# Optimization experiments

Hardware: AMD Instinct MI355X
Metric: run time of the kernel (lower is better)

The kernel has to match this reference:

```python
import jax, jax.numpy as jnp
import numpy as np
import math

B, N, E, F_IN, H = 16, 2048, 32768, 32, 128
RATIO = 0.8
K1 = math.ceil(RATIO * N)      # 1639
K2 = math.ceil(RATIO * K1)     # 1312
K3 = math.ceil(RATIO * K2)     # 1050


def setup_inputs() -> dict:
    key = jax.random.key(0)
    ks = jax.random.split(key, 20)

    def lin(k, out_d, in_d):
        s = 1.0 / np.sqrt(in_d)
        return jax.random.uniform(k, (out_d, in_d), minval=-s, maxval=s, dtype=jnp.float32)

    return {
        "x": jax.random.normal(ks[0], (B, N, F_IN), dtype=jnp.float32),
        "edge_index": jax.random.randint(ks[1], (B, 2, E), 0, N, dtype=jnp.int32),
        "W_root1": lin(ks[2], H, F_IN), "W_rel1": lin(ks[3], H, F_IN), "b1": jnp.zeros((H,), jnp.float32),
        "p1": jax.random.normal(ks[4], (H,), dtype=jnp.float32) * 0.1,
        "W_root2": lin(ks[5], H, H), "W_rel2": lin(ks[6], H, H), "b2": jnp.zeros((H,), jnp.float32),
        "p2": jax.random.normal(ks[7], (H,), dtype=jnp.float32) * 0.1,
        "W_root3": lin(ks[8], H, H), "W_rel3": lin(ks[9], H, H), "b3": jnp.zeros((H,), jnp.float32),
        "p3": jax.random.normal(ks[10], (H,), dtype=jnp.float32) * 0.1,
        "lin1_W": lin(ks[11], 128, 256), "lin1_b": jnp.zeros((128,), jnp.float32),
        "lin2_W": lin(ks[12], 64, 128), "lin2_b": jnp.zeros((64,), jnp.float32),
        "lin3_W": lin(ks[13], 1, 64), "lin3_b": jnp.zeros((1,), jnp.float32),
    }


def _graph_conv(x, src, dst, ev, W_rel, b, W_root):
    # GraphConv: out_i = W_root x_i + W_rel * sum_{j->i} x_j + b
    n = x.shape[0]
    msg = x[src] * ev[:, None].astype(x.dtype)            # [E, F] gather
    agg = jnp.zeros((n, x.shape[1]), x.dtype).at[dst].add(msg)  # scatter-add
    return agg @ W_rel.T + b + x @ W_root.T


def _topk_pool(x, src, dst, ev, p, k):
    # TopKPooling: score = tanh(x.p/||p||); keep top-k nodes; x' = x[perm]*score[perm]
    score = jnp.tanh((x @ p) / jnp.linalg.norm(p))        # [n]
    vals, perm = jax.lax.top_k(score, k)
    x_new = x[perm] * vals[:, None]
    inv = jnp.full((x.shape[0],), -1, jnp.int32).at[perm].set(jnp.arange(k, dtype=jnp.int32))
    ns, nd = inv[src], inv[dst]
    valid = ev & (ns >= 0) & (nd >= 0)
    return x_new, jnp.where(valid, ns, 0), jnp.where(valid, nd, 0), valid


def _readout(x):
    # cat([global_max_pool, global_mean_pool])
    return jnp.concatenate([x.max(axis=0), x.mean(axis=0)])


def reference(x, edge_index,
              W_root1, W_rel1, b1, p1,
              W_root2, W_rel2, b2, p2,
              W_root3, W_rel3, b3, p3,
              lin1_W, lin1_b, lin2_W, lin2_b, lin3_W, lin3_b):
    def per_graph(xg, eg):
        src, dst = eg[0], eg[1]
        ev = jnp.ones((E,), bool)
        h = jax.nn.relu(_graph_conv(xg, src, dst, ev, W_rel1, b1, W_root1))
        h, src, dst, ev = _topk_pool(h, src, dst, ev, p1, K1)
        r1 = _readout(h)
        h = jax.nn.relu(_graph_conv(h, src, dst, ev, W_rel2, b2, W_root2))
        h, src, dst, ev = _topk_pool(h, src, dst, ev, p2, K2)
        r2 = _readout(h)
        h = jax.nn.relu(_graph_conv(h, src, dst, ev, W_rel3, b3, W_root3))
        h, src, dst, ev = _topk_pool(h, src, dst, ev, p3, K3)
        r3 = _readout(h)
        return r1 + r2 + r3                                # [256]

    g = jax.vmap(per_graph)(x, edge_index)                 # [B, 256]
    h = jax.nn.relu(g @ lin1_W.T + lin1_b)
    h = jax.nn.relu(h @ lin2_W.T + lin2_b)
    out = jax.nn.sigmoid(h @ lin3_W.T + lin3_b)            # [B, 1]
    return out[:, 0]
```

## Files before the change

### kernel.cpp

```cpp
#include <hip/hip_runtime.h>
#include <cstdint>
#include <math.h>

#define BB 16
#define NN 2048
#define EE 32768
#define FIN 32
#define HH 128
#define KK1 1639
#define KK2 1312
#define KK3 1050
#define PARTS 128
#define PGRP 8
#define JPG (PARTS / PGRP)
#define DEGC 64

using f16x8 = __attribute__((ext_vector_type(8))) _Float16;
using f16x2 = __attribute__((ext_vector_type(2))) _Float16;
using f32x4 = __attribute__((ext_vector_type(4))) float;

__global__ void wcvt_kernel(const float* __restrict__ Wr1, const float* __restrict__ Wl1,
                            const float* __restrict__ Wr2, const float* __restrict__ Wl2,
                            const float* __restrict__ Wr3, const float* __restrict__ Wl3,
                            _Float16* __restrict__ wcat1, _Float16* __restrict__ wcat2,
                            _Float16* __restrict__ wcat3) {
    int idx = blockIdx.x * 256 + threadIdx.x;
    if (idx < 128 * 64) {
        int col = idx >> 6, k = idx & 63;
        float v = (k < FIN) ? Wr1[col * FIN + k] : Wl1[col * FIN + (k - FIN)];
        wcat1[idx] = (_Float16)v;
    } else if (idx < 128 * 64 + 128 * 256) {
        int i2 = idx - 128 * 64;
        int col = i2 >> 8, k = i2 & 255;
        float v = (k < HH) ? Wr2[col * HH + k] : Wl2[col * HH + (k - HH)];
        wcat2[i2] = (_Float16)v;
    } else {
        int i3 = idx - 128 * 64 - 128 * 256;
        if (i3 < 128 * 256) {
            int col = i3 >> 8, k = i3 & 255;
            float v = (k < HH) ? Wr3[col * HH + k] : Wl3[col * HH + (k - HH)];
            wcat3[i3] = (_Float16)v;
        }
    }
}

__global__ void build1_kernel(const int* __restrict__ ei,
                              int* __restrict__ deg, int* __restrict__ csr) {
    int t = blockIdx.x * blockDim.x + threadIdx.x;
    int e = t & (EE - 1);
    int b = t >> 15;
    if (b >= BB) return;
    int s = ei[(size_t)b * 2 * EE + e];
    int d = ei[(size_t)b * 2 * EE + EE + e];
    int pos = atomicAdd(&deg[b * NN + d], 1);
    if (pos < DEGC) csr[((size_t)b * NN + d) * DEGC + pos] = s;
}

__global__ __launch_bounds__(256) void agg1_csr_kernel(
    const float* __restrict__ x, const int* __restrict__ deg,
    const int* __restrict__ csr, _Float16* __restrict__ agg) {
    int b = blockIdx.x;
    int g = threadIdx.x >> 5, lane = threadIdx.x & 31;
    int node = blockIdx.y * 8 + g;
    int dg = deg[b * NN + node]; if (dg > DEGC) dg = DEGC;
    const int* bucket = csr + ((size_t)b * NN + node) * DEGC;
    float acc = 0.f;
    for (int base = 0; base < dg; base += 16) {
        int m = dg - base; if (m > 16) m = 16;
        int myidx = (lane < m) ? bucket[base + lane] : 0;
        float v[16];
        int idx[16];
#pragma unroll
        for (int u = 0; u < 16; u++) idx[u] = __shfl(myidx, u, 32);
#pragma unroll
        for (int u = 0; u < 16; u++)
            v[u] = x[((size_t)b * NN + idx[u]) * FIN + lane];
#pragma unroll
        for (int u = 0; u < 16; u++)
            acc += (u < m) ? v[u] : 0.f;
    }
    agg[((size_t)b * NN + node) * FIN + lane] = (_Float16)acc;
}

__global__ __launch_bounds__(256) void agg23_csr_kernel(
    const _Float16* __restrict__ x, const int* __restrict__ deg,
    const int* __restrict__ csr, _Float16* __restrict__ agg, int n) {
    int b = blockIdx.x;
    int wv = threadIdx.x >> 6, lane = threadIdx.x & 63;
    int node = blockIdx.y * 4 + wv;
    if (node >= n) return;
    int dg = deg[b * NN + node]; if (dg > DEGC) dg = DEGC;
    const int* bucket = csr + ((size_t)b * NN + node) * DEGC;
    const f16x2* xf2 = reinterpret_cast<const f16x2*>(x);
    float ax = 0.f, ay = 0.f;
    for (int base = 0; base < dg; base += 16) {
        int m = dg - base; if (m > 16) m = 16;
        int myidx = (lane < m) ? bucket[base + lane] : 0;
        int idx[16];
#pragma unroll
        for (int u = 0; u < 16; u++) idx[u] = __shfl(myidx, u);
        f16x2 v[16];
#pragma unroll
        for (int u = 0; u < 16; u++)
            v[u] = xf2[((size_t)b * NN + idx[u]) * 64 + lane];
#pragma unroll
        for (int u = 0; u < 16; u++) {
            ax += (u < m) ? (float)v[u][0] : 0.f;
            ay += (u < m) ? (float)v[u][1] : 0.f;
        }
    }
    f16x2 o; o[0] = (_Float16)ax; o[1] = (_Float16)ay;
    reinterpret_cast<f16x2*>(agg)[((size_t)b * NN + node) * 64 + lane] = o;
}

__device__ __forceinline__ f16x8 load_cvt16(const float* src) {
    float4 lo = *reinterpret_cast<const float4*>(src);
    float4 hi = *reinterpret_cast<const float4*>(src + 4);
    f16x8 r;
    r[0] = (_Float16)lo.x; r[1] = (_Float16)lo.y;
    r[2] = (_Float16)lo.z; r[3] = (_Float16)lo.w;
    r[4] = (_Float16)hi.x; r[5] = (_Float16)hi.y;
    r[6] = (_Float16)hi.z; r[7] = (_Float16)hi.w;
    return r;
}

template<int FI, bool XF32>
__global__ __launch_bounds__(256) void conv_mfma_kernel(
    const void* __restrict__ xv, const _Float16* __restrict__ ah,
    const _Float16* __restrict__ wcat,
    const float* __restrict__ bias, const float* __restrict__ p,
    _Float16* __restrict__ h, unsigned long long* __restrict__ keys,
    float* __restrict__ ssc, int n) {
    __shared__ float spart[4][32];
    __shared__ float snorm_s;
    const float* xf = (const float*)xv;
    const _Float16* xh = (const _Float16*)xv;
    int b = blockIdx.x;
    int r0 = blockIdx.y * 32;
    int t = threadIdx.x;
    int wv = t >> 6, lane = t & 63;
    int m16 = lane & 15, q = lane >> 4;

    if (t < 64) {
        float v = p[t] * p[t] + p[t + 64] * p[t + 64];
#pragma unroll
        for (int off = 32; off; off >>= 1) v += __shfl_xor(v, off);
        if (t == 0) snorm_s = sqrtf(v);
    }

    f32x4 acc[2][2];
#pragma unroll
    for (int rt = 0; rt < 2; rt++)
#pragma unroll
        for (int ct = 0; ct < 2; ct++) {
            acc[rt][ct][0] = 0.f; acc[rt][ct][1] = 0.f;
            acc[rt][ct][2] = 0.f; acc[rt][ct][3] = 0.f;
        }

    int rowA[2] = { r0 + m16, r0 + 16 + m16 };
    int colB[2] = { wv * 32 + m16, wv * 32 + 16 + m16 };

#pragma unroll
    for (int step = 0; step < (2 * FI) / 32; step++) {
        int k0 = step * 32 + q * 8;
        f16x8 afr[2], bfr[2];
#pragma unroll
        for (int rt = 0; rt < 2; rt++) {
            if (k0 < FI) {
                if constexpr (XF32)
                    afr[rt] = load_cvt16(xf + ((size_t)b * NN + rowA[rt]) * FI + k0);
                else
                    afr[rt] = *reinterpret_cast<const f16x8*>(
                        xh + ((size_t)b * NN + rowA[rt]) * FI + k0);
            } else {
                afr[rt] = *reinterpret_cast<const f16x8*>(
                    ah + ((size_t)b * NN + rowA[rt]) * FI + (k0 - FI));
            }
        }
#pragma unroll
        for (int ct = 0; ct < 2; ct++)
            bfr[ct] = *reinterpret_cast<const f16x8*>(
                wcat + (size_t)colB[ct] * (2 * FI) + k0);
#pragma unroll
        for (int rt = 0; rt < 2; rt++)
#pragma unroll
            for (int ct = 0; ct < 2; ct++)
                acc[rt][ct] = __builtin_amdgcn_mfma_f32_16x16x32_f16(
                    afr[rt], bfr[ct], acc[rt][ct], 0, 0, 0);
    }

    float prt[2][4];
#pragma unroll
    for (int rt = 0; rt < 2; rt++)
#pragma unroll
        for (int reg = 0; reg < 4; reg++) prt[rt][reg] = 0.f;

#pragma unroll
    for (int ct = 0; ct < 2; ct++) {
        int col = wv * 32 + ct * 16 + m16;
        float pc = p[col];
        float bv = bias[col];
#pragma unroll
        for (int rt = 0; rt < 2; rt++)
#pragma unroll
            for (int reg = 0; reg < 4; reg++) {
                int row = r0 + rt * 16 + q * 4 + reg;
                float hv = fmaxf(acc[rt][ct][reg] + bv, 0.f);
                if (row < n)
                    h[((size_t)b * NN + row) * HH + col] = (_Float16)hv;
                prt[rt][reg] += hv * pc;
            }
    }
#pragma unroll
    for (int rt = 0; rt < 2; rt++)
#pragma unroll
        for (int reg = 0; reg < 4; reg++) {
            float v = prt[rt][reg];
            v += __shfl_xor(v, 1); v += __shfl_xor(v, 2);
            v += __shfl_xor(v, 4); v += __shfl_xor(v, 8);
            prt[rt][reg] = v;
        }
    if (m16 == 0) {
#pragma unroll
        for (int rt = 0; rt < 2; rt++)
#pragma unroll
            for (int reg = 0; reg < 4; reg++)
                spart[wv][rt * 16 + q * 4 + reg] = prt[rt][reg];
    }
    __syncthreads();
    if (t < 32) {
        int row = r0 + t;
        if (row < n) {
            float s = spart[0][t] + spart[1][t] + spart[2][t] + spart[3][t];
            float sc = tanhf(s / snorm_s);
            unsigned u = __float_as_uint(sc);
            u = (u & 0x80000000u) ? ~u : (u ^ 0x80000000u);
            u = ~u;
            keys[(size_t)b * NN + row] = ((unsigned long long)u << 32) | (unsigned)row;
            ssc[(size_t)b * NN + row] = sc;
        }
    }
}

__global__ __launch_bounds__(256) void rank_kernel(
    const unsigned long long* __restrict__ keys, const float* __restrict__ ssc,
    int n, int k, int* __restrict__ perm, float* __restrict__ vals,
    int* __restrict__ inv) {
    __shared__ unsigned long long sk[NN];
    __shared__ int pr2[256];
    int b = blockIdx.x;
    for (int i = threadIdx.x; i < NN; i += 256)
        sk[i] = (i < n) ? keys[(size_t)b * NN + i] : ~0ULL;
    __syncthreads();
    int il = threadIdx.x & 63;
    int jg = threadIdx.x >> 6;
    int i = blockIdx.y * 64 + il;
    unsigned long long my = sk[i];
    int rank = 0;
#pragma unroll 8
    for (int j = jg * 512; j < jg * 512 + 512; j++)
        rank += (sk[j] < my) ? 1 : 0;
    pr2[threadIdx.x] = rank;
    __syncthreads();
    if (jg == 0 && i < n) {
        rank = pr2[il] + pr2[64 + il] + pr2[128 + il] + pr2[192 + il];
        if (rank < k) {
            perm[b * NN + rank] = i;
            vals[b * NN + rank] = ssc[(size_t)b * NN + i];
            inv[b * NN + i] = rank;
        } else {
            inv[b * NN + i] = -1;
        }
    }
}

__global__ __launch_bounds__(256) void fat_gather_build_kernel(
    int nbuild,
    const int* __restrict__ inv,
    const int* __restrict__ sin_, const int* __restrict__ din_, int in_stride,
    int* __restrict__ sout, int* __restrict__ dout, int write_next,
    int* __restrict__ deg, int* __restrict__ csr,
    const _Float16* __restrict__ hin, _Float16* __restrict__ xout,
    const int* __restrict__ perm, const float* __restrict__ vals, int k,
    float* __restrict__ part) {
    if ((int)blockIdx.x < nbuild) {
        int t = blockIdx.x * 256 + threadIdx.x;
        int e = t & (EE - 1);
        int b = t >> 15;
        if (b >= BB) return;
        int s = sin_[(size_t)b * in_stride + e];
        int d = din_[(size_t)b * in_stride + e];
        int ns = -1, nd = -1;
        if (s >= 0 && d >= 0) {
            ns = inv[b * NN + s];
            nd = inv[b * NN + d];
        }
        if (ns < 0 || nd < 0) { ns = -1; nd = -1; }
        if (write_next) {
            sout[(size_t)b * EE + e] = ns;
            dout[(size_t)b * EE + e] = nd;
        }
        if (nd >= 0) {
            int pos = atomicAdd(&deg[b * NN + nd], 1);
            if (pos < DEGC) csr[((size_t)b * NN + nd) * DEGC + pos] = ns;
        }
    } else {
        int gblk = blockIdx.x - nbuild;
        int pair = gblk * 2 + (threadIdx.x >> 7);
        int b = pair & 15;
        int j = pair >> 4;
        int f = threadIdx.x & 127;
        float mx = -INFINITY, sm = 0.f;
        int i = j;
        int pi = (i < k) ? perm[b * NN + i] : 0;
        float v = (i < k) ? vals[b * NN + i] : 0.f;
        while (i < k) {
            int inext = i + PARTS;
            int pin = 0; float vn = 0.f;
            if (inext < k) { pin = perm[b * NN + inext]; vn = vals[b * NN + inext]; }
            float hv = (float)hin[((size_t)b * NN + pi) * HH + f] * v;
            xout[((size_t)b * NN + i) * HH + f] = (_Float16)hv;
            mx = fmaxf(mx, hv);
            sm += hv;
            i = inext; pi = pin; v = vn;
        }
        part[((size_t)b * PARTS + j) * 256 + f] = mx;
        part[((size_t)b * PARTS + j) * 256 + 128 + f] = sm;
    }
}

__global__ __launch_bounds__(256) void combine_kernel(
    const float* __restrict__ partAll, float* __restrict__ partG) {
    int blk = blockIdx.x;
    int g = blk % PGRP;
    int rem = blk / PGRP;
    int b = rem & 15;
    int l = rem >> 4;
    int f = threadIdx.x;
    const float* src = partAll + ((((size_t)l * BB + b) * PARTS) + (size_t)g * JPG) * 256;
    float r;
    if (f < 128) {
        r = -INFINITY;
#pragma unroll
        for (int j = 0; j < JPG; j++) r = fmaxf(r, src[j * 256 + f]);
    } else {
        r = 0.f;
#pragma unroll
        for (int j = 0; j < JPG; j++) r += src[j * 256 + f];
    }
    partG[(((size_t)l * BB + b) * PGRP + g) * 256 + f] = r;
}

__global__ __launch_bounds__(256) void mlp_kernel(
    const float* __restrict__ partG,
    const float* __restrict__ W1, const float* __restrict__ b1,
    const float* __restrict__ W2, const float* __restrict__ b2,
    const float* __restrict__ W3, const float* __restrict__ b3,
    float* __restrict__ out) {
    __shared__ float sg[256];
    __shared__ float s1[128];
    __shared__ float s2[64];
    int b = blockIdx.x, tid = threadIdx.x;
    const float kk[3] = {(float)KK1, (float)KK2, (float)KK3};
    float acc = 0.f;
    if (tid < 128) {
#pragma unroll
        for (int l = 0; l < 3; l++) {
            float mx = -INFINITY;
#pragma unroll
            for (int j = 0; j < PGRP; j++)
                mx = fmaxf(mx, partG[(((size_t)l * BB + b) * PGRP + j) * 256 + tid]);
            acc += mx;
        }
    } else {
#pragma unroll
        for (int l = 0; l < 3; l++) {
            float sm = 0.f;
#pragma unroll
            for (int j = 0; j < PGRP; j++)
                sm += partG[(((size_t)l * BB + b) * PGRP + j) * 256 + tid];
            acc += sm / kk[l];
        }
    }
    sg[tid] = acc;
    __syncthreads();
    if (tid < 128) {
        float a = b1[tid];
        for (int j = 0; j < 256; j++) a += sg[j] * W1[tid * 256 + j];
        s1[tid] = fmaxf(a, 0.f);
    }
    __syncthreads();
    if (tid < 64) {
        float a = b2[tid];
        for (int j = 0; j < 128; j++) a += s1[j] * W2[tid * 128 + j];
        s2[tid] = fmaxf(a, 0.f);
    }
    __syncthreads();
    if (tid == 0) {
        float a = b3[0];
        for (int j = 0; j < 64; j++) a += s2[j] * W3[j];
        out[b] = 1.f / (1.f + expf(-a));
    }
}

extern "C" void kernel_launch(void* const* d_in, const int* in_sizes, int n_in,
                              void* d_out, int out_size, void* d_ws, size_t ws_size,
                              hipStream_t stream) {
    const float* x   = (const float*)d_in[0];
    const int*   ei  = (const int*)d_in[1];
    const float* Wr1 = (const float*)d_in[2];
    const float* Wl1 = (const float*)d_in[3];
    const float* b1  = (const float*)d_in[4];
    const float* p1  = (const float*)d_in[5];
    const float* Wr2 = (const float*)d_in[6];
    const float* Wl2 = (const float*)d_in[7];
    const float* b2  = (const float*)d_in[8];
    const float* p2  = (const float*)d_in[9];
    const float* Wr3 = (const float*)d_in[10];
    const float* Wl3 = (const float*)d_in[11];
    const float* b3  = (const float*)d_in[12];
    const float* p3  = (const float*)d_in[13];
    const float* l1W = (const float*)d_in[14];
    const float* l1b = (const float*)d_in[15];
    const float* l2W = (const float*)d_in[16];
    const float* l2b = (const float*)d_in[17];
    const float* l3W = (const float*)d_in[18];
    const float* l3b = (const float*)d_in[19];
    float* out = (float*)d_out;

    char* ws = (char*)d_ws;
    _Float16* bufA = (_Float16*)ws; ws += (size_t)BB * NN * HH * 2;
    _Float16* bufB = (_Float16*)ws; ws += (size_t)BB * NN * HH * 2;
    _Float16* agg  = (_Float16*)ws; ws += (size_t)BB * NN * HH * 2;
    int*   perm = (int*)ws;   ws += (size_t)BB * NN * 4;
    float* vals = (float*)ws; ws += (size_t)BB * NN * 4;
    int*   inv  = (int*)ws;   ws += (size_t)BB * NN * 4;
    int*   curS = (int*)ws;   ws += (size_t)BB * EE * 4;
    int*   curD = (int*)ws;   ws += (size_t)BB * EE * 4;
    float* partAll = (float*)ws; ws += (size_t)3 * BB * PARTS * 256 * 4;
    float* partG   = (float*)ws; ws += (size_t)3 * BB * PGRP * 256 * 4;
    int*   deg1 = (int*)ws;   ws += (size_t)BB * NN * 4;
    int*   deg2 = (int*)ws;   ws += (size_t)BB * NN * 4;
    int*   deg3 = (int*)ws;   ws += (size_t)BB * NN * 4;
    int*   csr  = (int*)ws;   ws += (size_t)BB * NN * DEGC * 4;
    unsigned long long* keys = (unsigned long long*)ws; ws += (size_t)BB * NN * 8;
    float* ssc  = (float*)ws; ws += (size_t)BB * NN * 4;
    _Float16* wcat1 = (_Float16*)ws; ws += (size_t)128 * 64 * 2;
    _Float16* wcat2 = (_Float16*)ws; ws += (size_t)128 * 256 * 2;
    _Float16* wcat3 = (_Float16*)ws; ws += (size_t)128 * 256 * 2;
    float* part1 = partAll;
    float* part2 = partAll + (size_t)BB * PARTS * 256;
    float* part3 = partAll + (size_t)2 * BB * PARTS * 256;

    hipMemsetAsync(deg1, 0, (size_t)3 * BB * NN * 4, stream);
    hipLaunchKernelGGL(wcvt_kernel, dim3((128 * 64 + 2 * 128 * 256 + 255) / 256), dim3(256), 0, stream,
                       Wr1, Wl1, Wr2, Wl2, Wr3, Wl3, wcat1, wcat2, wcat3);

    hipLaunchKernelGGL(build1_kernel, dim3(BB * EE / 256), dim3(256), 0, stream, ei, deg1, csr);
    hipLaunchKernelGGL(agg1_csr_kernel, dim3(BB, NN / 8), dim3(256), 0, stream, x, deg1, csr, agg);
    hipLaunchKernelGGL((conv_mfma_kernel<FIN, true>), dim3(BB, NN / 32), dim3(256), 0, stream,
                       (const void*)x, agg, wcat1, b1, p1, bufA, keys, ssc, NN);
    hipLaunchKernelGGL(rank_kernel, dim3(BB, NN / 64), dim3(256), 0, stream, keys, ssc, NN, KK1, perm, vals, inv);
    hipLaunchKernelGGL(fat_gather_build_kernel, dim3(2048 + BB * PARTS / 2), dim3(256), 0, stream,
                       2048, inv, ei, ei + EE, 2 * EE, curS, curD, 1, deg2, csr,
                       bufA, bufB, perm, vals, KK1, part1);

    hipLaunchKernelGGL(agg23_csr_kernel, dim3(BB, (KK1 + 3) / 4), dim3(256), 0, stream, bufB, deg2, csr, agg, KK1);
    hipLaunchKernelGGL((conv_mfma_kernel<HH, false>), dim3(BB, (KK1 + 31) / 32), dim3(256), 0, stream,
                       (const void*)bufB, agg, wcat2, b2, p2, bufA, keys, ssc, KK1);
    hipLaunchKernelGGL(rank_kernel, dim3(BB, NN / 64), dim3(256), 0, stream, keys, ssc, KK1, KK2, perm, vals, inv);
    hipLaunchKernelGGL(fat_gather_build_kernel, dim3(2048 + BB * PARTS / 2), dim3(256), 0, stream,
                       2048, inv, curS, curD, EE, curS, curD, 0, deg3, csr,
                       bufA, bufB, perm, vals, KK2, part2);

    hipLaunchKernelGGL(agg23_csr_kernel, dim3(BB, (KK2 + 3) / 4), dim3(256), 0, stream, bufB, deg3, csr, agg, KK2);
    hipLaunchKernelGGL((conv_mfma_kernel<HH, false>), dim3(BB, (KK2 + 31) / 32), dim3(256), 0, stream,
                       (const void*)bufB, agg, wcat3, b3, p3, bufA, keys, ssc, KK2);
    hipLaunchKernelGGL(rank_kernel, dim3(BB, NN / 64), dim3(256), 0, stream, keys, ssc, KK2, KK3, perm, vals, inv);
    hipLaunchKernelGGL(fat_gather_build_kernel, dim3(BB * PARTS / 2), dim3(256), 0, stream,
                       0, inv, curS, curD, EE, curS, curD, 0, deg3, csr,
                       bufA, bufB, perm, vals, KK3, part3);

    hipLaunchKernelGGL(combine_kernel, dim3(3 * BB * PGRP), dim3(256), 0, stream, partAll, partG);
    hipLaunchKernelGGL(mlp_kernel, dim3(BB), dim3(256), 0, stream,
                       partG, l1W, l1b, l2W, l2b, l3W, l3b, out);
}
```

Measured before the change: 217.5 us.

## Fuse CSR aggregation into MFMA conv kernels and merge prep launches

Neighbour aggregation now runs inside the conv kernels and writes into shared memory instead of a global agg buffer, so the separate agg kernels and their global round trip go away. The weight conversion and CSR build are merged into one prep kernel, and the combine kernel is dropped, so the MLP kernel reduces all 128 partials directly. This cuts launch count and global traffic. In exchange, the conv blocks become serial gather-then-MFMA with fewer blocks doing the gather work, and the MLP kernel now runs a longer serial reduction with only 16 blocks.

```diff
diff --git a/kernel.cpp b/kernel.cpp
--- a/kernel.cpp
+++ b/kernel.cpp
@@ -11,106 +11,48 @@
 #define KK2 1312
 #define KK3 1050
 #define PARTS 128
-#define PGRP 8
-#define JPG (PARTS / PGRP)
 #define DEGC 64
 
 using f16x8 = __attribute__((ext_vector_type(8))) _Float16;
 using f16x2 = __attribute__((ext_vector_type(2))) _Float16;
 using f32x4 = __attribute__((ext_vector_type(4))) float;
 
-__global__ void wcvt_kernel(const float* __restrict__ Wr1, const float* __restrict__ Wl1,
+__global__ void prep_kernel(const int* __restrict__ ei,
+                            int* __restrict__ deg, int* __restrict__ csr,
+                            const float* __restrict__ Wr1, const float* __restrict__ Wl1,
                             const float* __restrict__ Wr2, const float* __restrict__ Wl2,
                             const float* __restrict__ Wr3, const float* __restrict__ Wl3,
                             _Float16* __restrict__ wcat1, _Float16* __restrict__ wcat2,
                             _Float16* __restrict__ wcat3) {
-    int idx = blockIdx.x * 256 + threadIdx.x;
-    if (idx < 128 * 64) {
-        int col = idx >> 6, k = idx & 63;
-        float v = (k < FIN) ? Wr1[col * FIN + k] : Wl1[col * FIN + (k - FIN)];
-        wcat1[idx] = (_Float16)v;
-    } else if (idx < 128 * 64 + 128 * 256) {
-        int i2 = idx - 128 * 64;
-        int col = i2 >> 8, k = i2 & 255;
-        float v = (k < HH) ? Wr2[col * HH + k] : Wl2[col * HH + (k - HH)];
-        wcat2[i2] = (_Float16)v;
+    if (blockIdx.x < 2048) {
+        int t = blockIdx.x * 256 + threadIdx.x;
+        int e = t & (EE - 1);
+        int b = t >> 15;
+        if (b >= BB) return;
+        int s = ei[(size_t)b * 2 * EE + e];
+        int d = ei[(size_t)b * 2 * EE + EE + e];
+        int pos = atomicAdd(&deg[b * NN + d], 1);
+        if (pos < DEGC) csr[((size_t)b * NN + d) * DEGC + pos] = s;
     } else {
-        int i3 = idx - 128 * 64 - 128 * 256;
-        if (i3 < 128 * 256) {
-            int col = i3 >> 8, k = i3 & 255;
-            float v = (k < HH) ? Wr3[col * HH + k] : Wl3[col * HH + (k - HH)];
-            wcat3[i3] = (_Float16)v;
-        }
-    }
-}
-
-__global__ void build1_kernel(const int* __restrict__ ei,
-                              int* __restrict__ deg, int* __restrict__ csr) {
-    int t = blockIdx.x * blockDim.x + threadIdx.x;
-    int e = t & (EE - 1);
-    int b = t >> 15;
-    if (b >= BB) return;
-    int s = ei[(size_t)b * 2 * EE + e];
-    int d = ei[(size_t)b * 2 * EE + EE + e];
-    int pos = atomicAdd(&deg[b * NN + d], 1);
-    if (pos < DEGC) csr[((size_t)b * NN + d) * DEGC + pos] = s;
-}
-
-__global__ __launch_bounds__(256) void agg1_csr_kernel(
-    const float* __restrict__ x, const int* __restrict__ deg,
-    const int* __restrict__ csr, _Float16* __restrict__ agg) {
-    int b = blockIdx.x;
-    int g = threadIdx.x >> 5, lane = threadIdx.x & 31;
-    int node = blockIdx.y * 8 + g;
-    int dg = deg[b * NN + node]; if (dg > DEGC) dg = DEGC;
-    const int* bucket = csr + ((size_t)b * NN + node) * DEGC;
-    float acc = 0.f;
-    for (int base = 0; base < dg; base += 16) {
-        int m = dg - base; if (m > 16) m = 16;
-        int myidx = (lane < m) ? bucket[base + lane] : 0;
-        float v[16];
-        int idx[16];
-#pragma unroll
-        for (int u = 0; u < 16; u++) idx[u] = __shfl(myidx, u, 32);
-#pragma unroll
-        for (int u = 0; u < 16; u++)
-            v[u] = x[((size_t)b * NN + idx[u]) * FIN + lane];
-#pragma unroll
-        for (int u = 0; u < 16; u++)
-            acc += (u < m) ? v[u] : 0.f;
-    }
-    agg[((size_t)b * NN + node) * FIN + lane] = (_Float16)acc;
-}
-
-__global__ __launch_bounds__(256) void agg23_csr_kernel(
-    const _Float16* __restrict__ x, const int* __restrict__ deg,
-    const int* __restrict__ csr, _Float16* __restrict__ agg, int n) {
-    int b = blockIdx.x;
-    int wv = threadIdx.x >> 6, lane = threadIdx.x & 63;
-    int node = blockIdx.y * 4 + wv;
-    if (node >= n) return;
-    int dg = deg[b * NN + node]; if (dg > DEGC) dg = DEGC;
-    const int* bucket = csr + ((size_t)b * NN + node) * DEGC;
-    const f16x2* xf2 = reinterpret_cast<const f16x2*>(x);
-    float ax = 0.f, ay = 0.f;
-    for (int base = 0; base < dg; base += 16) {
-        int m = dg - base; if (m > 16) m = 16;
-        int myidx = (lane < m) ? bucket[base + lane] : 0;
-        int idx[16];
-#pragma unroll
-        for (int u = 0; u < 16; u++) idx[u] = __shfl(myidx, u);
-        f16x2 v[16];
-#pragma unroll
-        for (int u = 0; u < 16; u++)
-            v[u] = xf2[((size_t)b * NN + idx[u]) * 64 + lane];
-#pragma unroll
-        for (int u = 0; u < 16; u++) {
-            ax += (u < m) ? (float)v[u][0] : 0.f;
-            ay += (u < m) ? (float)v[u][1] : 0.f;
-        }
-    }
-    f16x2 o; o[0] = (_Float16)ax; o[1] = (_Float16)ay;
-    reinterpret_cast<f16x2*>(agg)[((size_t)b * NN + node) * 64 + lane] = o;
+        int idx = (blockIdx.x - 2048) * 256 + threadIdx.x;
+        if (idx < 128 * 64) {
+            int col = idx >> 6, k = idx & 63;
+            float v = (k < FIN) ? Wr1[col * FIN + k] : Wl1[col * FIN + (k - FIN)];
+            wcat1[idx] = (_Float16)v;
+        } else if (idx < 128 * 64 + 128 * 256) {
+            int i2 = idx - 128 * 64;
+            int col = i2 >> 8, k = i2 & 255;
+            float v = (k < HH) ? Wr2[col * HH + k] : Wl2[col * HH + (k - HH)];
+            wcat2[i2] = (_Float16)v;
+        } else {
+            int i3 = idx - 128 * 64 - 128 * 256;
+            if (i3 < 128 * 256) {
+                int col = i3 >> 8, k = i3 & 255;
+                float v = (k < HH) ? Wr3[col * HH + k] : Wl3[col * HH + (k - HH)];
+                wcat3[i3] = (_Float16)v;
+            }
+        }
+    }
 }
 
 __device__ __forceinline__ f16x8 load_cvt16(const float* src) {
@@ -124,22 +66,154 @@
     return r;
 }
 
-template<int FI, bool XF32>
-__global__ __launch_bounds__(256) void conv_mfma_kernel(
-    const void* __restrict__ xv, const _Float16* __restrict__ ah,
-    const _Float16* __restrict__ wcat,
+__global__ __launch_bounds__(256) void convagg1_kernel(
+    const float* __restrict__ x, const int* __restrict__ deg,
+    const int* __restrict__ csr, const _Float16* __restrict__ wcat,
     const float* __restrict__ bias, const float* __restrict__ p,
     _Float16* __restrict__ h, unsigned long long* __restrict__ keys,
     float* __restrict__ ssc, int n) {
+    __shared__ _Float16 sagg[32][40];
     __shared__ float spart[4][32];
     __shared__ float snorm_s;
-    const float* xf = (const float*)xv;
-    const _Float16* xh = (const _Float16*)xv;
+    int b = blockIdx.x;
+    int r0 = blockIdx.y * 32;
+    int t = threadIdx.x;
+
+    if (t < 64) {
+        float v = p[t] * p[t] + p[t + 64] * p[t + 64];
+#pragma unroll
+        for (int off = 32; off; off >>= 1) v += __shfl_xor(v, off);
+        if (t == 0) snorm_s = sqrtf(v);
+    }
+
+    {
+        int g = t >> 5, lane = t & 31;
+#pragma unroll
+        for (int nl = 0; nl < 4; nl++) {
+            int nloc = g * 4 + nl;
+            int node = r0 + nloc;
+            int dg = deg[b * NN + node]; if (dg > DEGC) dg = DEGC;
+            const int* bucket = csr + ((size_t)b * NN + node) * DEGC;
+            float acc = 0.f;
+            for (int base = 0; base < dg; base += 16) {
+                int m = dg - base; if (m > 16) m = 16;
+                int myidx = (lane < m) ? bucket[base + lane] : 0;
+                int idx[16];
+#pragma unroll
+                for (int u = 0; u < 16; u++) idx[u] = __shfl(myidx, u, 32);
+                float v[16];
+#pragma unroll
+                for (int u = 0; u < 16; u++)
+                    v[u] = x[((size_t)b * NN + idx[u]) * FIN + lane];
+#pragma unroll
+                for (int u = 0; u < 16; u++)
+                    acc += (u < m) ? v[u] : 0.f;
+            }
+            sagg[nloc][lane] = (_Float16)acc;
+        }
+    }
+    __syncthreads();
+
+    int wv = t >> 6, lane = t & 63;
+    int m16 = lane & 15, q = lane >> 4;
+    f32x4 acc[2][2];
+#pragma unroll
+    for (int rt = 0; rt < 2; rt++)
+#pragma unroll
+        for (int ct = 0; ct < 2; ct++) {
+            acc[rt][ct][0] = 0.f; acc[rt][ct][1] = 0.f;
+            acc[rt][ct][2] = 0.f; acc[rt][ct][3] = 0.f;
+        }
+    int rowL[2] = { m16, 16 + m16 };
+    int colB[2] = { wv * 32 + m16, wv * 32 + 16 + m16 };
+
+#pragma unroll
+    for (int step = 0; step < 2; step++) {
+        int k0 = step * 32 + q * 8;
+        f16x8 afr[2], bfr[2];
+#pragma unroll
+        for (int rt = 0; rt < 2; rt++) {
+            if (k0 < FIN)
+                afr[rt] = load_cvt16(x + ((size_t)b * NN + r0 + rowL[rt]) * FIN + k0);
+            else
+                afr[rt] = *reinterpret_cast<const f16x8*>(&sagg[rowL[rt]][k0 - FIN]);
+        }
+#pragma unroll
+        for (int ct = 0; ct < 2; ct++)
+            bfr[ct] = *reinterpret_cast<const f16x8*>(wcat + (size_t)colB[ct] * 64 + k0);
+#pragma unroll
+        for (int rt = 0; rt < 2; rt++)
+#pragma unroll
+            for (int ct = 0; ct < 2; ct++)
+                acc[rt][ct] = __builtin_amdgcn_mfma_f32_16x16x32_f16(
+                    afr[rt], bfr[ct], acc[rt][ct], 0, 0, 0);
+    }
+
+    float prt[2][4];
+#pragma unroll
+    for (int rt = 0; rt < 2; rt++)
+#pragma unroll
+        for (int reg = 0; reg < 4; reg++) prt[rt][reg] = 0.f;
+#pragma unroll
+    for (int ct = 0; ct < 2; ct++) {
+        int col = wv * 32 + ct * 16 + m16;
+        float pc = p[col];
+        float bv = bias[col];
+#pragma unroll
+        for (int rt = 0; rt < 2; rt++)
+#pragma unroll
+            for (int reg = 0; reg < 4; reg++) {
+                int row = r0 + rt * 16 + q * 4 + reg;
+                float hv = fmaxf(acc[rt][ct][reg] + bv, 0.f);
+                if (row < n)
+                    h[((size_t)b * NN + row) * HH + col] = (_Float16)hv;
+                prt[rt][reg] += hv * pc;
+            }
+    }
+#pragma unroll
+    for (int rt = 0; rt < 2; rt++)
+#pragma unroll
+        for (int reg = 0; reg < 4; reg++) {
+            float v = prt[rt][reg];
+            v += __shfl_xor(v, 1); v += __shfl_xor(v, 2);
+            v += __shfl_xor(v, 4); v += __shfl_xor(v, 8);
+            prt[rt][reg] = v;
+        }
+    if (m16 == 0) {
+#pragma unroll
+        for (int rt = 0; rt < 2; rt++)
+#pragma unroll
+            for (int reg = 0; reg < 4; reg++)
+                spart[wv][rt * 16 + q * 4 + reg] = prt[rt][reg];
+    }
+    __syncthreads();
+    if (t < 32) {
+        int row = r0 + t;
+        if (row < n) {
+            float s = spart[0][t] + spart[1][t] + spart[2][t] + spart[3][t];
+            float sc = tanhf(s / snorm_s);
+            unsigned u = __float_as_uint(sc);
+            u = (u & 0x80000000u) ? ~u : (u ^ 0x80000000u);
+            u = ~u;
+            keys[(size_t)b * NN + row] = ((unsigned long long)u << 32) | (unsigned)row;
+            ssc[(size_t)b * NN + row] = sc;
+        }
+    }
+}
+
+__global__ __launch_bounds__(256) void convagg23_kernel(
+    const _Float16* __restrict__ x, const int* __restrict__ deg,
+    const int* __restrict__ csr, const _Float16* __restrict__ wcat,
+    const float* __restrict__ bias, const float* __restrict__ p,
+    _Float16* __restrict__ h, unsigned long long* __restrict__ keys,
+    float* __restrict__ ssc, int n) {
+    __shared__ _Float16 sagg[32][136];
+    __shared__ float spart[4][32];
+    __shared__ float snorm_s;
     int b = blockIdx.x;
     int r0 = blockIdx.y * 32;
     int t = threadIdx.x;
     int wv = t >> 6, lane = t & 63;
-    int m16 = lane & 15, q = lane >> 4;
 
     if (t < 64) {
         float v = p[t] * p[t] + p[t + 64] * p[t + 64];
@@ -148,6 +222,39 @@
         if (t == 0) snorm_s = sqrtf(v);
     }
 
+    {
+        const f16x2* xf2 = reinterpret_cast<const f16x2*>(x);
+#pragma unroll
+        for (int nl = 0; nl < 8; nl++) {
+            int nloc = wv * 8 + nl;
+            int node = r0 + nloc;
+            int dg = (node < n) ? deg[b * NN + node] : 0;
+            if (dg > DEGC) dg = DEGC;
+            const int* bucket = csr + ((size_t)b * NN + node) * DEGC;
+            float ax = 0.f, ay = 0.f;
+            for (int base = 0; base < dg; base += 16) {
+                int m = dg - base; if (m > 16) m = 16;
+                int myidx = (lane < m) ? bucket[base + lane] : 0;
+                int idx[16];
+#pragma unroll
+                for (int u = 0; u < 16; u++) idx[u] = __shfl(myidx, u);
+                f16x2 v[16];
+#pragma unroll
+                for (int u = 0; u < 16; u++)
+                    v[u] = xf2[((size_t)b * NN + idx[u]) * 64 + lane];
+#pragma unroll
+                for (int u = 0; u < 16; u++) {
+                    ax += (u < m) ? (float)v[u][0] : 0.f;
+                    ay += (u < m) ? (float)v[u][1] : 0.f;
+                }
+            }
+            sagg[nloc][lane * 2]     = (_Float16)ax;
+            sagg[nloc][lane * 2 + 1] = (_Float16)ay;
+        }
+    }
+    __syncthreads();
+
+    int m16 = lane & 15, q = lane >> 4;
     f32x4 acc[2][2];
 #pragma unroll
     for (int rt = 0; rt < 2; rt++)
@@ -156,31 +263,24 @@
             acc[rt][ct][0] = 0.f; acc[rt][ct][1] = 0.f;
             acc[rt][ct][2] = 0.f; acc[rt][ct][3] = 0.f;
         }
-
-    int rowA[2] = { r0 + m16, r0 + 16 + m16 };
+    int rowL[2] = { m16, 16 + m16 };
     int colB[2] = { wv * 32 + m16, wv * 32 + 16 + m16 };
 
 #pragma unroll
-    for (int step = 0; step < (2 * FI) / 32; step++) {
+    for (int step = 0; step < 8; step++) {
         int k0 = step * 32 + q * 8;
         f16x8 afr[2], bfr[2];
 #pragma unroll
         for (int rt = 0; rt < 2; rt++) {
-            if (k0 < FI) {
-                if constexpr (XF32)
-                    afr[rt] = load_cvt16(xf + ((size_t)b * NN + rowA[rt]) * FI + k0);
-                else
-                    afr[rt] = *reinterpret_cast<const f16x8*>(
-                        xh + ((size_t)b * NN + rowA[rt]) * FI + k0);
-            } else {
+            if (k0 < HH)
                 afr[rt] = *reinterpret_cast<const f16x8*>(
-                    ah + ((size_t)b * NN + rowA[rt]) * FI + (k0 - FI));
-            }
+                    x + ((size_t)b * NN + r0 + rowL[rt]) * HH + k0);
+            else
+                afr[rt] = *reinterpret_cast<const f16x8*>(&sagg[rowL[rt]][k0 - HH]);
         }
 #pragma unroll
         for (int ct = 0; ct < 2; ct++)
-            bfr[ct] = *reinterpret_cast<const f16x8*>(
-                wcat + (size_t)colB[ct] * (2 * FI) + k0);
+            bfr[ct] = *reinterpret_cast<const f16x8*>(wcat + (size_t)colB[ct] * 256 + k0);
 #pragma unroll
         for (int rt = 0; rt < 2; rt++)
 #pragma unroll
@@ -194,7 +294,6 @@
     for (int rt = 0; rt < 2; rt++)
 #pragma unroll
         for (int reg = 0; reg < 4; reg++) prt[rt][reg] = 0.f;
-
 #pragma unroll
     for (int ct = 0; ct < 2; ct++) {
         int col = wv * 32 + ct * 16 + m16;
@@ -329,30 +428,8 @@
     }
 }
 
-__global__ __launch_bounds__(256) void combine_kernel(
-    const float* __restrict__ partAll, float* __restrict__ partG) {
-    int blk = blockIdx.x;
-    int g = blk % PGRP;
-    int rem = blk / PGRP;
-    int b = rem & 15;
-    int l = rem >> 4;
-    int f = threadIdx.x;
-    const float* src = partAll + ((((size_t)l * BB + b) * PARTS) + (size_t)g * JPG) * 256;
-    float r;
-    if (f < 128) {
-        r = -INFINITY;
-#pragma unroll
-        for (int j = 0; j < JPG; j++) r = fmaxf(r, src[j * 256 + f]);
-    } else {
-        r = 0.f;
-#pragma unroll
-        for (int j = 0; j < JPG; j++) r += src[j * 256 + f];
-    }
-    partG[(((size_t)l * BB + b) * PGRP + g) * 256 + f] = r;
-}
-
 __global__ __launch_bounds__(256) void mlp_kernel(
-    const float* __restrict__ partG,
+    const float* __restrict__ partAll,
     const float* __restrict__ W1, const float* __restrict__ b1,
     const float* __restrict__ W2, const float* __restrict__ b2,
     const float* __restrict__ W3, const float* __restrict__ b3,
@@ -367,18 +444,18 @@
 #pragma unroll
         for (int l = 0; l < 3; l++) {
             float mx = -INFINITY;
-#pragma unroll
-            for (int j = 0; j < PGRP; j++)
-                mx = fmaxf(mx, partG[(((size_t)l * BB + b) * PGRP + j) * 256 + tid]);
+#pragma unroll 4
+            for (int j = 0; j < PARTS; j++)
+                mx = fmaxf(mx, partAll[(((size_t)l * BB + b) * PARTS + j) * 256 + tid]);
             acc += mx;
         }
     } else {
 #pragma unroll
         for (int l = 0; l < 3; l++) {
             float sm = 0.f;
-#pragma unroll
-            for (int j = 0; j < PGRP; j++)
-                sm += partG[(((size_t)l * BB + b) * PGRP + j) * 256 + tid];
+#pragma unroll 4
+            for (int j = 0; j < PARTS; j++)
+                sm += partAll[(((size_t)l * BB + b) * PARTS + j) * 256 + tid];
             acc += sm / kk[l];
         }
     }
@@ -431,14 +508,12 @@
     char* ws = (char*)d_ws;
     _Float16* bufA = (_Float16*)ws; ws += (size_t)BB * NN * HH * 2;
     _Float16* bufB = (_Float16*)ws; ws += (size_t)BB * NN * HH * 2;
-    _Float16* agg  = (_Float16*)ws; ws += (size_t)BB * NN * HH * 2;
     int*   perm = (int*)ws;   ws += (size_t)BB * NN * 4;
     float* vals = (float*)ws; ws += (size_t)BB * NN * 4;
     int*   inv  = (int*)ws;   ws += (size_t)BB * NN * 4;
     int*   curS = (int*)ws;   ws += (size_t)BB * EE * 4;
     int*   curD = (int*)ws;   ws += (size_t)BB * EE * 4;
     float* partAll = (float*)ws; ws += (size_t)3 * BB * PARTS * 256 * 4;
-    float* partG   = (float*)ws; ws += (size_t)3 * BB * PGRP * 256 * 4;
     int*   deg1 = (int*)ws;   ws += (size_t)BB * NN * 4;
     int*   deg2 = (int*)ws;   ws += (size_t)BB * NN * 4;
     int*   deg3 = (int*)ws;   ws += (size_t)BB * NN * 4;
@@ -453,35 +528,30 @@
     float* part3 = partAll + (size_t)2 * BB * PARTS * 256;
 
     hipMemsetAsync(deg1, 0, (size_t)3 * BB * NN * 4, stream);
-    hipLaunchKernelGGL(wcvt_kernel, dim3((128 * 64 + 2 * 128 * 256 + 255) / 256), dim3(256), 0, stream,
-                       Wr1, Wl1, Wr2, Wl2, Wr3, Wl3, wcat1, wcat2, wcat3);
-
-    hipLaunchKernelGGL(build1_kernel, dim3(BB * EE / 256), dim3(256), 0, stream, ei, deg1, csr);
-    hipLaunchKernelGGL(agg1_csr_kernel, dim3(BB, NN / 8), dim3(256), 0, stream, x, deg1, csr, agg);
-    hipLaunchKernelGGL((conv_mfma_kernel<FIN, true>), dim3(BB, NN / 32), dim3(256), 0, stream,
-                       (const void*)x, agg, wcat1, b1, p1, bufA, keys, ssc, NN);
+    hipLaunchKernelGGL(prep_kernel, dim3(2048 + (128 * 64 + 2 * 128 * 256 + 255) / 256), dim3(256), 0, stream,
+                       ei, deg1, csr, Wr1, Wl1, Wr2, Wl2, Wr3, Wl3, wcat1, wcat2, wcat3);
+
+    hipLaunchKernelGGL(convagg1_kernel, dim3(BB, NN / 32), dim3(256), 0, stream,
+                       x, deg1, csr, wcat1, b1, p1, bufA, keys, ssc, NN);
     hipLaunchKernelGGL(rank_kernel, dim3(BB, NN / 64), dim3(256), 0, stream, keys, ssc, NN, KK1, perm, vals, inv);
     hipLaunchKernelGGL(fat_gather_build_kernel, dim3(2048 + BB * PARTS / 2), dim3(256), 0, stream,
                        2048, inv, ei, ei + EE, 2 * EE, curS, curD, 1, deg2, csr,
                        bufA, bufB, perm, vals, KK1, part1);
 
-    hipLaunchKernelGGL(agg23_csr_kernel, dim3(BB, (KK1 + 3) / 4), dim3(256), 0, stream, bufB, deg2, csr, agg, KK1);
-    hipLaunchKernelGGL((conv_mfma_kernel<HH, false>), dim3(BB, (KK1 + 31) / 32), dim3(256), 0, stream,
-                       (const void*)bufB, agg, wcat2, b2, p2, bufA, keys, ssc, KK1);
+    hipLaunchKernelGGL(convagg23_kernel, dim3(BB, (KK1 + 31) / 32), dim3(256), 0, stream,
+                       bufB, deg2, csr, wcat2, b2, p2, bufA, keys, ssc, KK1);
     hipLaunchKernelGGL(rank_kernel, dim3(BB, NN / 64), dim3(256), 0, stream, keys, ssc, KK1, KK2, perm, vals, inv);
     hipLaunchKernelGGL(fat_gather_build_kernel, dim3(2048 + BB * PARTS / 2), dim3(256), 0, stream,
                        2048, inv, curS, curD, EE, curS, curD, 0, deg3, csr,
                        bufA, bufB, perm, vals, KK2, part2);
 
-    hipLaunchKernelGGL(agg23_csr_kernel, dim3(BB, (KK2 + 3) / 4), dim3(256), 0, stream, bufB, deg3, csr, agg, KK2);
-    hipLaunchKernelGGL((conv_mfma_kernel<HH, false>), dim3(BB, (KK2 + 31) / 32), dim3(256), 0, stream,
-                       (const void*)bufB, agg, wcat3, b3, p3, bufA, keys, ssc, KK2);
+    hipLaunchKernelGGL(convagg23_kernel, dim3(BB, (KK2 + 31) / 32), dim3(256), 0, stream,
+                       bufB, deg3, csr, wcat3, b3, p3, bufA, keys, ssc, KK2);
     hipLaunchKernelGGL(rank_kernel, dim3(BB, NN / 64), dim3(256), 0, stream, keys, ssc, KK2, KK3, perm, vals, inv);
     hipLaunchKernelGGL(fat_gather_build_kernel, dim3(BB * PARTS / 2), dim3(256), 0, stream,
                        0, inv, curS, curD, EE, curS, curD, 0, deg3, csr,
                        bufA, bufB, perm, vals, KK3, part3);
 
-    hipLaunchKernelGGL(combine_kernel, dim3(3 * BB * PGRP), dim3(256), 0, stream, partAll, partG);
     hipLaunchKernelGGL(mlp_kernel, dim3(BB), dim3(256), 0, stream,
-                       partG, l1W, l1b, l2W, l2b, l3W, l3b, out);
-}
+                       partAll, l1W, l1b, l2W, l2b, l3W, l3b, out);
+}
```

Result: slower. 266.5 us (+22.6%).
